# Kernel optimization log

Hardware: AMD Instinct MI355X
Metric: run time of the kernel (lower is better)

The kernel has to match this reference:

```python
import jax, jax.numpy as jnp
import numpy as np

NUM_HEADS = 16
HEAD_DIM = 64
EMBED_DIM = NUM_HEADS * HEAD_DIM  # 1024


def setup_inputs() -> dict:
    key = jax.random.key(0)
    k1, k2, k3 = jax.random.split(key, 3)
    B, T, C = 4, 2048, EMBED_DIM
    x = jax.random.normal(k1, (B, T, C), dtype=jnp.float32)
    # Linear weights stored [in, out] so y = x @ W (== torch x @ W.T with torch layout)
    w_qkv = jax.random.normal(k2, (C, 3 * C), dtype=jnp.float32) * (1.0 / np.sqrt(C))
    w_out = jax.random.normal(k3, (C, C), dtype=jnp.float32) * (1.0 / np.sqrt(C))
    return {"x": x, "w_qkv": w_qkv, "w_out": w_out}


def reference(x, w_qkv, w_out):
    B, T, C = x.shape
    H, D = NUM_HEADS, HEAD_DIM
    scale = 1.0 / jnp.sqrt(jnp.asarray(D, dtype=x.dtype))

    qkv = x @ w_qkv  # [B, T, 3C]
    q, k, v = jnp.split(qkv, 3, axis=-1)

    def split_heads(t):
        return t.reshape(B, T, H, D).transpose(0, 2, 1, 3)  # [B, H, T, D]

    q, k, v = split_heads(q), split_heads(k), split_heads(v)

    scores = jnp.einsum("bhqd,bhkd->bhqk", q, k) * scale  # [B, H, T, T]
    causal = jnp.tril(jnp.ones((T, T), dtype=bool))
    scores = jnp.where(causal, scores, -jnp.inf)
    weights = jax.nn.softmax(scores, axis=-1)
    out = jnp.einsum("bhqk,bhkd->bhqd", weights, v)  # [B, H, T, D]
    out = out.transpose(0, 2, 1, 3).reshape(B, T, C)
    return out @ w_out
```

## Files before the change

kernel.cpp:

```cpp
#include <hip/hip_runtime.h>

typedef __attribute__((ext_vector_type(8))) short bf16x8;
typedef __attribute__((ext_vector_type(4))) float f32x4;
typedef __attribute__((ext_vector_type(8))) unsigned short u16x8;

#define USHORT unsigned short

__device__ __forceinline__ USHORT f2bf(float f){
  unsigned int u = __builtin_bit_cast(unsigned int, f);
  u = (u + 0x7FFFu + ((u >> 16) & 1u)) >> 16;
  return (USHORT)u;
}

__device__ __forceinline__ void gl_lds16(const void* g, void* l){
  __builtin_amdgcn_global_load_lds((const __attribute__((address_space(1))) void*)g,
                                   (__attribute__((address_space(3))) void*)l, 16, 0, 0);
}

__global__ __launch_bounds__(256) void cvt_x(const float* __restrict__ x,
                                             USHORT* __restrict__ xb){
  int i = blockIdx.x * 256 + threadIdx.x;
  const float4* p = (const float4*)x;
  float4 a = p[i*2], b = p[i*2+1];
  u16x8 v;
  v[0]=f2bf(a.x); v[1]=f2bf(a.y); v[2]=f2bf(a.z); v[3]=f2bf(a.w);
  v[4]=f2bf(b.x); v[5]=f2bf(b.y); v[6]=f2bf(b.z); v[7]=f2bf(b.w);
  ((u16x8*)xb)[i] = v;
}

__global__ __launch_bounds__(256) void transpose_f32_bf16(const float* __restrict__ src,
                                                          USHORT* __restrict__ dst,
                                                          int rows, int cols){
  __shared__ USHORT t[32][33];
  int x0 = blockIdx.x * 32, y0 = blockIdx.y * 32;
  int tx = threadIdx.x, ty = threadIdx.y;
  #pragma unroll
  for (int i=0;i<4;i++)
    t[ty+i*8][tx] = f2bf(src[(size_t)(y0+ty+i*8)*cols + x0+tx]);
  __syncthreads();
  #pragma unroll
  for (int i=0;i<4;i++)
    dst[(size_t)(x0+ty+i*8)*rows + y0+tx] = t[tx][ty+i*8];
}

__global__ __launch_bounds__(256) void transpose_v(const USHORT* __restrict__ V,
                                                   USHORT* __restrict__ VT){
  __shared__ USHORT t[32][33];
  int bh = blockIdx.z;
  const USHORT* src = V + (size_t)bh*2048*64;
  USHORT* dst = VT + (size_t)bh*64*2048;
  int x0 = blockIdx.x * 32;
  int y0 = blockIdx.y * 32;
  int tx = threadIdx.x, ty = threadIdx.y;
  #pragma unroll
  for (int i=0;i<4;i++)
    t[ty+i*8][tx] = src[(size_t)(y0+ty+i*8)*64 + x0+tx];
  __syncthreads();
  #pragma unroll
  for (int i=0;i<4;i++)
    dst[(size_t)(x0+ty+i*8)*2048 + y0+tx] = t[tx][ty+i*8];
}

template<int EPI>
__global__ __launch_bounds__(256) void gemm_bt(
    const USHORT* __restrict__ A, const USHORT* __restrict__ Bt,
    float* __restrict__ Cf,
    USHORT* __restrict__ Qo, USHORT* __restrict__ Ko, USHORT* __restrict__ Vo,
    int M, int N, int K)
{
  __shared__ USHORT As[128*32];
  __shared__ USHORT Bs[128*32];
  const int tid = threadIdx.x;
  const int lane = tid & 63, li = lane & 15, g = lane >> 4;
  const int wv = tid >> 6, wr = wv >> 1, wc = wv & 1;
  const int m0 = blockIdx.y * 128, n0 = blockIdx.x * 128;

  f32x4 acc[4][4];
  #pragma unroll
  for (int m=0;m<4;m++)
    #pragma unroll
    for (int n=0;n<4;n++) acc[m][n] = (f32x4){0.f,0.f,0.f,0.f};

  for (int kk = 0; kk < K; kk += 32){
    __syncthreads();
    #pragma unroll
    for (int it=0; it<2; ++it){
      int c = it*256 + tid;
      int row = c >> 2, sl = c & 3;
      gl_lds16(A  + (size_t)(m0+row)*K + kk + sl*8, &As[c*8]);
      gl_lds16(Bt + (size_t)(n0+row)*K + kk + sl*8, &Bs[c*8]);
    }
    __syncthreads();
    bf16x8 af[4], bfr[4];
    #pragma unroll
    for (int m=0;m<4;m++) af[m]  = *(const bf16x8*)&As[(wr*64+m*16+li)*32 + g*8];
    #pragma unroll
    for (int n=0;n<4;n++) bfr[n] = *(const bf16x8*)&Bs[(wc*64+n*16+li)*32 + g*8];
    #pragma unroll
    for (int m=0;m<4;m++)
      #pragma unroll
      for (int n=0;n<4;n++)
        acc[m][n] = __builtin_amdgcn_mfma_f32_16x16x32_bf16(af[m], bfr[n], acc[m][n], 0,0,0);
  }

  if (EPI == 0){
    #pragma unroll
    for (int m=0;m<4;m++)
      #pragma unroll
      for (int n=0;n<4;n++){
        int col  = n0 + wc*64 + n*16 + li;
        int rowb = m0 + wr*64 + m*16 + g*4;
        #pragma unroll
        for (int r=0;r<4;r++)
          Cf[(size_t)(rowb+r)*N + col] = acc[m][n][r];
      }
  } else {
    #pragma unroll
    for (int m=0;m<4;m++)
      #pragma unroll
      for (int n=0;n<4;n++){
        int col = n0 + wc*64 + n*16 + li;
        int which = col >> 10, hd = col & 1023, h = hd >> 6, d = hd & 63;
        USHORT* dst = (which==0) ? Qo : ((which==1) ? Ko : Vo);
        float sc = (which==0) ? 0.125f : 1.0f;
        int rowb = m0 + wr*64 + m*16 + g*4;
        #pragma unroll
        for (int r=0;r<4;r++){
          int grow = rowb + r;
          int b = grow >> 11, t = grow & 2047;
          dst[((size_t)(b*16+h)*2048 + t)*64 + d] = f2bf(acc[m][n][r]*sc);
        }
      }
  }
}

__global__ __launch_bounds__(256) void attn_kern(
    const USHORT* __restrict__ Q, const USHORT* __restrict__ Kc,
    const USHORT* __restrict__ VT, USHORT* __restrict__ Aout)
{
  __shared__ USHORT Pl[4][32*64];
  const int qt = 15 - blockIdx.x;
  const int bh = blockIdx.y;
  const int q0 = qt * 128;
  const int tid = threadIdx.x, lane = tid & 63, li = lane & 15, g = lane >> 4;
  const int wv = tid >> 6;
  const USHORT* Qb = Q  + (size_t)bh*2048*64;
  const USHORT* Kb = Kc + (size_t)bh*2048*64;
  const USHORT* Vb = VT + (size_t)bh*64*2048;
  char* pw = (char*)&Pl[wv][0];

  bf16x8 aq[2][2];
  #pragma unroll
  for (int m=0;m<2;m++)
    #pragma unroll
    for (int ks=0;ks<2;ks++){
      int row = q0 + wv*32 + m*16 + li;
      aq[m][ks] = *(const bf16x8*)&Qb[(size_t)row*64 + ks*32 + g*8];
    }

  f32x4 o[2][4];
  float mrun[2][4], lrun[2][4];
  #pragma unroll
  for (int m=0;m<2;m++){
    #pragma unroll
    for (int n=0;n<4;n++) o[m][n] = (f32x4){0.f,0.f,0.f,0.f};
    #pragma unroll
    for (int r=0;r<4;r++){ mrun[m][r] = -1e30f; lrun[m][r] = 0.f; }
  }

  const int nkt = 2*qt + 2;
  for (int kt = 0; kt < nkt; ++kt){
    const USHORT* Kt = Kb + (size_t)kt*64*64;

    f32x4 s[2][4];
    #pragma unroll
    for (int m=0;m<2;m++)
      #pragma unroll
      for (int nf=0;nf<4;nf++){
        f32x4 z = (f32x4){0.f,0.f,0.f,0.f};
        #pragma unroll
        for (int ks=0;ks<2;ks++){
          bf16x8 bk = *(const bf16x8*)&Kt[(size_t)(nf*16+li)*64 + ks*32 + g*8];
          z = __builtin_amdgcn_mfma_f32_16x16x32_bf16(aq[m][ks], bk, z, 0,0,0);
        }
        s[m][nf] = z;
      }

    if (kt >= 2*qt){
      #pragma unroll
      for (int m=0;m<2;m++){
        int rowb = q0 + wv*32 + m*16 + g*4;
        #pragma unroll
        for (int nf=0;nf<4;nf++){
          int col = kt*64 + nf*16 + li;
          #pragma unroll
          for (int r=0;r<4;r++)
            if (col > rowb + r) s[m][nf][r] = -1e30f;
        }
      }
    }

    #pragma unroll
    for (int m=0;m<2;m++){
      #pragma unroll
      for (int r=0;r<4;r++){
        float v = s[m][0][r];
        #pragma unroll
        for (int nf=1;nf<4;nf++) v = fmaxf(v, s[m][nf][r]);
        #pragma unroll
        for (int d=1;d<16;d<<=1) v = fmaxf(v, __shfl_xor(v, d, 64));
        float mnew = fmaxf(mrun[m][r], v);
        float scale = __expf(mrun[m][r] - mnew);
        float psum = 0.f;
        #pragma unroll
        for (int nf=0;nf<4;nf++){
          float p = __expf(s[m][nf][r] - mnew);
          s[m][nf][r] = p;
          psum += p;
        }
        #pragma unroll
        for (int d=1;d<16;d<<=1) psum += __shfl_xor(psum, d, 64);
        lrun[m][r] = lrun[m][r]*scale + psum;
        mrun[m][r] = mnew;
        #pragma unroll
        for (int nd=0;nd<4;nd++) o[m][nd][r] *= scale;
      }
      #pragma unroll
      for (int nf=0;nf<4;nf++)
        #pragma unroll
        for (int r=0;r<4;r++){
          int q = m*16 + g*4 + r;
          int key = nf*16 + li;
          int addr = q*128 + ((key*2) ^ ((q & 7) << 4));
          *(USHORT*)(pw + addr) = f2bf(s[m][nf][r]);
        }
    }

    asm volatile("s_waitcnt lgkmcnt(0)" ::: "memory");
    __builtin_amdgcn_sched_barrier(0);

    #pragma unroll
    for (int m=0;m<2;m++){
      int prow = m*16 + li;
      int xorv = (prow & 7) << 4;
      #pragma unroll
      for (int ks=0;ks<2;ks++){
        bf16x8 pa = *(const bf16x8*)(pw + prow*128 + ((ks*64 + g*16) ^ xorv));
        #pragma unroll
        for (int nd=0;nd<4;nd++){
          bf16x8 vb = *(const bf16x8*)&Vb[(size_t)(nd*16+li)*2048 + kt*64 + ks*32 + g*8];
          o[m][nd] = __builtin_amdgcn_mfma_f32_16x16x32_bf16(pa, vb, o[m][nd], 0,0,0);
        }
      }
    }
  }

  const int b = bh >> 4, h = bh & 15;
  #pragma unroll
  for (int m=0;m<2;m++)
    #pragma unroll
    for (int nd=0;nd<4;nd++)
      #pragma unroll
      for (int r=0;r<4;r++){
        int t = q0 + wv*32 + m*16 + g*4 + r;
        int d = nd*16 + li;
        float val = o[m][nd][r] / lrun[m][r];
        Aout[((size_t)(b*2048 + t))*1024 + h*64 + d] = f2bf(val);
      }
}

extern "C" void kernel_launch(void* const* d_in, const int* in_sizes, int n_in,
                              void* d_out, int out_size, void* d_ws, size_t ws_size,
                              hipStream_t stream) {
  const float* x     = (const float*)d_in[0];
  const float* w_qkv = (const float*)d_in[1];
  const float* w_out = (const float*)d_in[2];
  float* out = (float*)d_out;
  char* ws = (char*)d_ws;

  USHORT* xb    = (USHORT*)(ws);
  USHORT* wqkvT = (USHORT*)(ws + 16777216);
  USHORT* woutT = (USHORT*)(ws + 23068672);
  USHORT* Qb    = (USHORT*)(ws + 25165824);
  USHORT* Kb    = (USHORT*)(ws + 41943040);
  USHORT* Vb    = (USHORT*)(ws + 58720256);
  USHORT* VT    = xb;
  USHORT* Aout  = Vb;

  cvt_x<<<4096, 256, 0, stream>>>(x, xb);
  transpose_f32_bf16<<<dim3(96,32), dim3(32,8), 0, stream>>>(w_qkv, wqkvT, 1024, 3072);
  transpose_f32_bf16<<<dim3(32,32), dim3(32,8), 0, stream>>>(w_out, woutT, 1024, 1024);
  gemm_bt<1><<<dim3(24,64), 256, 0, stream>>>(xb, wqkvT, nullptr, Qb, Kb, Vb, 8192, 3072, 1024);
  transpose_v<<<dim3(2,64,64), dim3(32,8), 0, stream>>>(Vb, VT);
  attn_kern<<<dim3(16,64), 256, 0, stream>>>(Qb, Kb, VT, Aout);
  gemm_bt<0><<<dim3(8,64), 256, 0, stream>>>(Aout, woutT, out, nullptr, nullptr, nullptr, 8192, 1024, 1024);
}
```

Before: 448.8 us.

## Rewrite attention inner loop with 32x32 MFMA, exp2 softmax and lazy rescale

The attention kernel now gives each wave 32 query rows and walks 32-key tiles using 32x32x16 bf16 MFMAs. It computes S^T so the row max and sum reduce with a single cross-half shuffle. Q is prescaled by log2(e)/8 so the softmax can use exp2, and the running-max rescale of the output is skipped while the max grows by no more than 8. K tiles are prefetched one iteration ahead, each wave gets an exact causal tile count, and packed bf16 conversion is used for P and the output. The lazy rescale lets unnormalized values grow by up to 2^8 in fp32 and bf16, which slightly changes numerics.

Measured after the change: 430.0 us. 4.2% less time.

```diff
diff --git a/kernel.cpp b/kernel.cpp
--- a/kernel.cpp
+++ b/kernel.cpp
@@ -2,7 +2,9 @@
 
 typedef __attribute__((ext_vector_type(8))) short bf16x8;
 typedef __attribute__((ext_vector_type(4))) float f32x4;
+typedef __attribute__((ext_vector_type(16))) float f32x16;
 typedef __attribute__((ext_vector_type(8))) unsigned short u16x8;
+typedef __attribute__((ext_vector_type(2))) int i32x2;
 
 #define USHORT unsigned short
 
@@ -16,6 +18,14 @@
   __builtin_amdgcn_global_load_lds((const __attribute__((address_space(1))) void*)g,
                                    (__attribute__((address_space(3))) void*)l, 16, 0, 0);
 }
+
+__device__ __forceinline__ int cvtpk(float lo, float hi){
+  int r;
+  asm("v_cvt_pk_bf16_f32 %0, %1, %2" : "=v"(r) : "v"(lo), "v"(hi));
+  return r;
+}
+
+__device__ __forceinline__ float sx32f(float v){ return __shfl_xor(v, 32, 64); }
 
 __global__ __launch_bounds__(256) void cvt_x(const float* __restrict__ x,
                                              USHORT* __restrict__ xb){
@@ -122,7 +132,7 @@
         int col = n0 + wc*64 + n*16 + li;
         int which = col >> 10, hd = col & 1023, h = hd >> 6, d = hd & 63;
         USHORT* dst = (which==0) ? Qo : ((which==1) ? Ko : Vo);
-        float sc = (which==0) ? 0.125f : 1.0f;
+        float sc = (which==0) ? 0.18033688f : 1.0f;
         int rowb = m0 + wr*64 + m*16 + g*4;
         #pragma unroll
         for (int r=0;r<4;r++){
@@ -138,135 +148,121 @@
     const USHORT* __restrict__ Q, const USHORT* __restrict__ Kc,
     const USHORT* __restrict__ VT, USHORT* __restrict__ Aout)
 {
-  __shared__ USHORT Pl[4][32*64];
+  __shared__ USHORT Pl[4][32*32];
   const int qt = 15 - blockIdx.x;
   const int bh = blockIdx.y;
-  const int q0 = qt * 128;
-  const int tid = threadIdx.x, lane = tid & 63, li = lane & 15, g = lane >> 4;
+  const int tid = threadIdx.x;
+  const int lane = tid & 63, l31 = lane & 31;
+  const int hi = lane >> 5;
   const int wv = tid >> 6;
+  const int qbase = qt*128 + wv*32;
+  const int nkt = 4*qt + wv + 1;
+  char* pw = (char*)&Pl[wv][0];
+  const int swz = ((l31 >> 1) & 3) << 4;
+
   const USHORT* Qb = Q  + (size_t)bh*2048*64;
   const USHORT* Kb = Kc + (size_t)bh*2048*64;
   const USHORT* Vb = VT + (size_t)bh*64*2048;
-  char* pw = (char*)&Pl[wv][0];
-
-  bf16x8 aq[2][2];
-  #pragma unroll
-  for (int m=0;m<2;m++)
+
+  const USHORT* Qlane = Qb + (size_t)(qbase + l31)*64 + hi*8;
+  const USHORT* Klane = Kb + (size_t)l31*64 + hi*8;
+  const USHORT* Vlane = Vb + (size_t)l31*2048 + hi*8;
+
+  bf16x8 qf[4];
+  #pragma unroll
+  for (int ks=0;ks<4;ks++) qf[ks] = *(const bf16x8*)(Qlane + ks*16);
+
+  f32x16 o0 = {}, o1 = {};
+  float mrun = -1e30f, lrun = 0.f;
+
+  bf16x8 kf[4];
+  #pragma unroll
+  for (int ks=0;ks<4;ks++) kf[ks] = *(const bf16x8*)(Klane + ks*16);
+
+  for (int kt = 0; kt < nkt; ++kt){
+    bf16x8 vf0[2], vf1[2];
     #pragma unroll
     for (int ks=0;ks<2;ks++){
-      int row = q0 + wv*32 + m*16 + li;
-      aq[m][ks] = *(const bf16x8*)&Qb[(size_t)row*64 + ks*32 + g*8];
-    }
-
-  f32x4 o[2][4];
-  float mrun[2][4], lrun[2][4];
-  #pragma unroll
-  for (int m=0;m<2;m++){
-    #pragma unroll
-    for (int n=0;n<4;n++) o[m][n] = (f32x4){0.f,0.f,0.f,0.f};
-    #pragma unroll
-    for (int r=0;r<4;r++){ mrun[m][r] = -1e30f; lrun[m][r] = 0.f; }
-  }
-
-  const int nkt = 2*qt + 2;
-  for (int kt = 0; kt < nkt; ++kt){
-    const USHORT* Kt = Kb + (size_t)kt*64*64;
-
-    f32x4 s[2][4];
-    #pragma unroll
-    for (int m=0;m<2;m++)
-      #pragma unroll
-      for (int nf=0;nf<4;nf++){
-        f32x4 z = (f32x4){0.f,0.f,0.f,0.f};
-        #pragma unroll
-        for (int ks=0;ks<2;ks++){
-          bf16x8 bk = *(const bf16x8*)&Kt[(size_t)(nf*16+li)*64 + ks*32 + g*8];
-          z = __builtin_amdgcn_mfma_f32_16x16x32_bf16(aq[m][ks], bk, z, 0,0,0);
-        }
-        s[m][nf] = z;
+      vf0[ks] = *(const bf16x8*)(Vlane + kt*32 + ks*16);
+      vf1[ks] = *(const bf16x8*)(Vlane + 32*2048 + kt*32 + ks*16);
+    }
+
+    f32x16 s = {};
+    #pragma unroll
+    for (int ks=0;ks<4;ks++)
+      s = __builtin_amdgcn_mfma_f32_32x32x16_bf16(kf[ks], qf[ks], s, 0,0,0);
+
+    int ktp = (kt+1 < nkt) ? kt+1 : kt;
+    bf16x8 kn[4];
+    #pragma unroll
+    for (int ks=0;ks<4;ks++)
+      kn[ks] = *(const bf16x8*)(Klane + (size_t)ktp*2048 + ks*16);
+
+    if (kt == nkt-1){
+      #pragma unroll
+      for (int r=0;r<16;r++){
+        int key = kt*32 + (r&3) + 8*(r>>2) + 4*hi;
+        if (key > qbase + l31) s[r] = -1e30f;
       }
-
-    if (kt >= 2*qt){
-      #pragma unroll
-      for (int m=0;m<2;m++){
-        int rowb = q0 + wv*32 + m*16 + g*4;
-        #pragma unroll
-        for (int nf=0;nf<4;nf++){
-          int col = kt*64 + nf*16 + li;
-          #pragma unroll
-          for (int r=0;r<4;r++)
-            if (col > rowb + r) s[m][nf][r] = -1e30f;
-        }
-      }
-    }
-
-    #pragma unroll
-    for (int m=0;m<2;m++){
-      #pragma unroll
-      for (int r=0;r<4;r++){
-        float v = s[m][0][r];
-        #pragma unroll
-        for (int nf=1;nf<4;nf++) v = fmaxf(v, s[m][nf][r]);
-        #pragma unroll
-        for (int d=1;d<16;d<<=1) v = fmaxf(v, __shfl_xor(v, d, 64));
-        float mnew = fmaxf(mrun[m][r], v);
-        float scale = __expf(mrun[m][r] - mnew);
-        float psum = 0.f;
-        #pragma unroll
-        for (int nf=0;nf<4;nf++){
-          float p = __expf(s[m][nf][r] - mnew);
-          s[m][nf][r] = p;
-          psum += p;
-        }
-        #pragma unroll
-        for (int d=1;d<16;d<<=1) psum += __shfl_xor(psum, d, 64);
-        lrun[m][r] = lrun[m][r]*scale + psum;
-        mrun[m][r] = mnew;
-        #pragma unroll
-        for (int nd=0;nd<4;nd++) o[m][nd][r] *= scale;
-      }
-      #pragma unroll
-      for (int nf=0;nf<4;nf++)
-        #pragma unroll
-        for (int r=0;r<4;r++){
-          int q = m*16 + g*4 + r;
-          int key = nf*16 + li;
-          int addr = q*128 + ((key*2) ^ ((q & 7) << 4));
-          *(USHORT*)(pw + addr) = f2bf(s[m][nf][r]);
-        }
-    }
-
+    }
+
+    float a0 = fmaxf(s[0],s[1]),  a1 = fmaxf(s[2],s[3]),  a2 = fmaxf(s[4],s[5]),  a3 = fmaxf(s[6],s[7]);
+    float a4 = fmaxf(s[8],s[9]),  a5 = fmaxf(s[10],s[11]),a6 = fmaxf(s[12],s[13]),a7 = fmaxf(s[14],s[15]);
+    float b0 = fmaxf(a0,a1), b1 = fmaxf(a2,a3), b2 = fmaxf(a4,a5), b3 = fmaxf(a6,a7);
+    float vmax = fmaxf(fmaxf(b0,b1), fmaxf(b2,b3));
+    float pmax = fmaxf(vmax, sx32f(vmax));
+
+    if (!__all(pmax - mrun <= 8.0f)){
+      float mnew = fmaxf(mrun, pmax);
+      float sc = __builtin_amdgcn_exp2f(mrun - mnew);
+      lrun *= sc;
+      #pragma unroll
+      for (int r=0;r<16;r++){ o0[r] *= sc; o1[r] *= sc; }
+      mrun = mnew;
+    }
+
+    #pragma unroll
+    for (int r=0;r<16;r++) s[r] = __builtin_amdgcn_exp2f(s[r] - mrun);
+
+    float c0 = (s[0]+s[1])+(s[2]+s[3]), c1 = (s[4]+s[5])+(s[6]+s[7]);
+    float c2 = (s[8]+s[9])+(s[10]+s[11]), c3 = (s[12]+s[13])+(s[14]+s[15]);
+    float vsum = (c0+c1)+(c2+c3);
+    lrun += vsum + sx32f(vsum);
+
+    #pragma unroll
+    for (int r=0;r<16;r+=2){
+      int key = (r&3) + 8*(r>>2) + 4*hi;
+      int w = cvtpk(s[r], s[r+1]);
+      *(int*)(pw + l31*64 + ((key*2) ^ swz)) = w;
+    }
     asm volatile("s_waitcnt lgkmcnt(0)" ::: "memory");
     __builtin_amdgcn_sched_barrier(0);
 
-    #pragma unroll
-    for (int m=0;m<2;m++){
-      int prow = m*16 + li;
-      int xorv = (prow & 7) << 4;
-      #pragma unroll
-      for (int ks=0;ks<2;ks++){
-        bf16x8 pa = *(const bf16x8*)(pw + prow*128 + ((ks*64 + g*16) ^ xorv));
-        #pragma unroll
-        for (int nd=0;nd<4;nd++){
-          bf16x8 vb = *(const bf16x8*)&Vb[(size_t)(nd*16+li)*2048 + kt*64 + ks*32 + g*8];
-          o[m][nd] = __builtin_amdgcn_mfma_f32_16x16x32_bf16(pa, vb, o[m][nd], 0,0,0);
-        }
-      }
-    }
-  }
-
+    bf16x8 pf0 = *(const bf16x8*)(pw + l31*64 + ((hi*16)      ^ swz));
+    bf16x8 pf1 = *(const bf16x8*)(pw + l31*64 + ((32 + hi*16) ^ swz));
+
+    o0 = __builtin_amdgcn_mfma_f32_32x32x16_bf16(vf0[0], pf0, o0, 0,0,0);
+    o0 = __builtin_amdgcn_mfma_f32_32x32x16_bf16(vf0[1], pf1, o0, 0,0,0);
+    o1 = __builtin_amdgcn_mfma_f32_32x32x16_bf16(vf1[0], pf0, o1, 0,0,0);
+    o1 = __builtin_amdgcn_mfma_f32_32x32x16_bf16(vf1[1], pf1, o1, 0,0,0);
+
+    #pragma unroll
+    for (int ks=0;ks<4;ks++) kf[ks] = kn[ks];
+  }
+
+  float rl = __builtin_amdgcn_rcpf(lrun);
   const int b = bh >> 4, h = bh & 15;
-  #pragma unroll
-  for (int m=0;m<2;m++)
-    #pragma unroll
-    for (int nd=0;nd<4;nd++)
-      #pragma unroll
-      for (int r=0;r<4;r++){
-        int t = q0 + wv*32 + m*16 + g*4 + r;
-        int d = nd*16 + li;
-        float val = o[m][nd][r] / lrun[m][r];
-        Aout[((size_t)(b*2048 + t))*1024 + h*64 + d] = f2bf(val);
-      }
+  USHORT* orow = Aout + ((size_t)(b*2048 + qbase + l31))*1024 + h*64;
+  #pragma unroll
+  for (int g4=0; g4<4; g4++){
+    i32x2 u0, u1;
+    u0[0] = cvtpk(o0[4*g4]*rl,   o0[4*g4+1]*rl);
+    u0[1] = cvtpk(o0[4*g4+2]*rl, o0[4*g4+3]*rl);
+    *(i32x2*)(orow + 8*g4 + 4*hi) = u0;
+    u1[0] = cvtpk(o1[4*g4]*rl,   o1[4*g4+1]*rl);
+    u1[1] = cvtpk(o1[4*g4+2]*rl, o1[4*g4+3]*rl);
+    *(i32x2*)(orow + 32 + 8*g4 + 4*hi) = u1;
+  }
 }
 
 extern "C" void kernel_launch(void* const* d_in, const int* in_sizes, int n_in,
```
